# Optimization experiments

Hardware: AMD Instinct MI355X
Metric: run time of the kernel (lower is better)

Reference implementation:

```python
import jax, jax.numpy as jnp
import numpy as np

EPS = 1e-5
TEMP = 0.07
LARGE_NEG = -1e9


def mi_net(x, W1, g1, b1, W2, b2, Ws, lng, lnb):
    # x: (B, C, T). 1x1 convs == per-position channel projections.
    y = jnp.einsum('bct,oc->bot', x, W1)                      # conv1 (no bias)
    mu = y.mean(axis=(0, 2), keepdims=True)                   # BatchNorm2d, training-mode batch stats
    var = y.var(axis=(0, 2), keepdims=True)
    y = (y - mu) * jax.lax.rsqrt(var + EPS) * g1[None, :, None] + b1[None, :, None]
    y = jax.nn.relu(y)
    y = jnp.einsum('bot,po->bpt', y, W2) + b2[None, :, None]  # conv2 (bias)
    h = y + jnp.einsum('bct,oc->bot', x, Ws)                  # linear shortcut
    mu2 = h.mean(axis=1, keepdims=True)                       # LayerNorm over channel dim
    v2 = h.var(axis=1, keepdims=True)
    return (h - mu2) * jax.lax.rsqrt(v2 + EPS) * lng[None, :, None] + lnb[None, :, None]


def infonce(L, G):
    # L: (N, D, T) locals, G: (N, D) single global per sample (n_multis = 1)
    N, D, T = L.shape
    l_p = jnp.swapaxes(L, 1, 2)                               # (N, T, D)
    l_p = l_p / jnp.linalg.norm(l_p, axis=2, keepdims=True)
    g = G / jnp.linalg.norm(G, axis=1, keepdims=True)         # (N, D)
    u_p = (jnp.einsum('ntd,nd->nt', l_p, g) / TEMP)[:, :, None]   # (N, T, 1), positives scaled by temp
    # negatives: <global_i, local_{j,t}>; NOT divided by temperature (faithful to torch source)
    u_n = jnp.einsum('nd,mtd->nmt', g, l_p)                   # (N, N, T)
    eye = jnp.eye(N, dtype=bool)[:, :, None]
    u_n = jnp.where(eye, LARGE_NEG, u_n).reshape(N, N * T)    # mask self pairs
    logits = jnp.concatenate(
        [u_p, jnp.broadcast_to(u_n[:, None, :], (N, T, N * T))], axis=2)  # (N, T, 1+N*T)
    logp = jax.nn.log_softmax(logits, axis=2)
    return -logp[:, :, 0].mean()


def setup_inputs() -> dict:
    key = jax.random.key(0)
    ks = jax.random.split(key, 10)
    B, CL, CG, T, MI = 32, 1536, 192, 256, 512
    d = {
        'local_feat': jax.random.normal(ks[0], (B, CL, T), jnp.float32),
        'global_feat': jax.random.normal(ks[1], (B, CG), jnp.float32),
        # local_net params
        'lW1': jax.random.normal(ks[2], (MI, CL), jnp.float32) * 0.02,
        'lg1': jnp.ones((MI,), jnp.float32),
        'lb1': jnp.zeros((MI,), jnp.float32),
        'lW2': jax.random.normal(ks[3], (MI, MI), jnp.float32) * 0.02,
        'lb2': jnp.zeros((MI,), jnp.float32),
        'lWs': jax.random.normal(ks[4], (MI, CL), jnp.float32) * 0.02,
        'llng': jnp.ones((MI,), jnp.float32),
        'llnb': jnp.zeros((MI,), jnp.float32),
        # global_net params (global_channels != mi_units -> net exists)
        'gW1': jax.random.normal(ks[5], (MI, CG), jnp.float32) * 0.02,
        'gg1': jnp.ones((MI,), jnp.float32),
        'gb1': jnp.zeros((MI,), jnp.float32),
        'gW2': jax.random.normal(ks[6], (MI, MI), jnp.float32) * 0.02,
        'gb2': jnp.zeros((MI,), jnp.float32),
    }
    # shortcut with near-identity init (n_units >= n_input for global net)
    gWs = jax.random.uniform(ks[7], (MI, CG), jnp.float32, -0.01, 0.01)
    gWs = gWs.at[jnp.arange(CG), jnp.arange(CG)].set(1.0)
    d['gWs'] = gWs
    d['glng'] = jnp.ones((MI,), jnp.float32)
    d['glnb'] = jnp.zeros((MI,), jnp.float32)
    return d


def reference(local_feat, global_feat,
              lW1, lg1, lb1, lW2, lb2, lWs, llng, llnb,
              gW1, gg1, gb1, gW2, gb2, gWs, glng, glnb):
    L = mi_net(local_feat, lW1, lg1, lb1, lW2, lb2, lWs, llng, llnb)      # (B, MI, T)
    G = mi_net(global_feat[:, :, None], gW1, gg1, gb1, gW2, gb2, gWs, glng, glnb)[:, :, 0]  # (B, MI)
    return infonce(L, G)
```

## Files before the change

kernel.cpp:

```cpp
#include <hip/hip_runtime.h>

#define B 32
#define CL 1536
#define CG 192
#define T 256
#define MI 512
#define NPOS 8192
#define EPS 1e-5f
#define TEMP 0.07f

typedef __attribute__((ext_vector_type(8))) __bf16 bf16x8;
typedef __attribute__((ext_vector_type(4))) float f32x4;

__device__ __forceinline__ unsigned short f2bf(float f) {
  union { float f; unsigned u; } v; v.f = f;
  unsigned r = v.u + 0x7FFFu + ((v.u >> 16) & 1u);
  return (unsigned short)(r >> 16);
}
__device__ __forceinline__ float bf2f(unsigned short h) {
  union { unsigned u; float f; } v; v.u = ((unsigned)h) << 16;
  return v.f;
}

__device__ __forceinline__ float wave_sum(float v) {
#pragma unroll
  for (int off = 32; off > 0; off >>= 1) v += __shfl_xor(v, off, 64);
  return v;
}
__device__ __forceinline__ float block_sum(float v, float* rb) {
  v = wave_sum(v);
  __syncthreads();
  if ((threadIdx.x & 63) == 0) rb[threadIdx.x >> 6] = v;
  __syncthreads();
  return rb[0] + rb[1] + rb[2] + rb[3];
}

__global__ __launch_bounds__(256) void k_prep(
    const float* __restrict__ x, const float* __restrict__ lW1,
    const float* __restrict__ lWs, const float* __restrict__ lW2,
    const float* __restrict__ gx, const float* __restrict__ gW1,
    unsigned short* __restrict__ xT, unsigned short* __restrict__ Wc,
    unsigned short* __restrict__ W2b, float* __restrict__ y1g,
    float* __restrict__ bsum) {
  __shared__ float xs[64][65];
  const int bi = blockIdx.x, tid = threadIdx.x;
  if (bi < 1792) {
    int idx = (bi * 256 + tid) * 4;
    const float* src; unsigned short* dst;
    if (idx < 786432) { src = lW1 + idx; dst = Wc + idx; }
    else if (idx < 1572864) { src = lWs + (idx - 786432); dst = Wc + idx; }
    else { src = lW2 + (idx - 1572864); dst = W2b + (idx - 1572864); }
    float4 v = *(const float4*)src;
    ushort4 o = {f2bf(v.x), f2bf(v.y), f2bf(v.z), f2bf(v.w)};
    *(ushort4*)dst = o;
  } else if (bi < 4864) {
    int bi2 = bi - 1792;
    int b = bi2 / 96, rem = bi2 - b * 96;
    int c0 = (rem >> 2) * 64, t0 = (rem & 3) * 64;
    const float* xb = x + ((size_t)b * CL + c0) * T + t0;
#pragma unroll
    for (int i = 0; i < 4; i++) {
      int idx = tid + i * 256, c = idx >> 4, t4 = idx & 15;
      float4 v = *(const float4*)&xb[(size_t)c * T + t4 * 4];
      xs[c][t4 * 4 + 0] = v.x;
      xs[c][t4 * 4 + 1] = v.y;
      xs[c][t4 * 4 + 2] = v.z;
      xs[c][t4 * 4 + 3] = v.w;
    }
    __syncthreads();
    unsigned short* ob = xT + ((size_t)b * T + t0) * CL + c0;
#pragma unroll
    for (int half = 0; half < 2; half++) {
      int s = tid + half * 256;
      int t = s >> 3, kg = s & 7;
      unsigned short v[8];
#pragma unroll
      for (int j = 0; j < 8; j++) v[j] = f2bf(xs[kg * 8 + j][t]);
      uint4 o = {(unsigned)v[0] | ((unsigned)v[1] << 16),
                 (unsigned)v[2] | ((unsigned)v[3] << 16),
                 (unsigned)v[4] | ((unsigned)v[5] << 16),
                 (unsigned)v[6] | ((unsigned)v[7] << 16)};
      *(uint4*)&ob[(size_t)t * CL + kg * 8] = o;
    }
  } else if (bi < 4928) {
    int idx = (bi - 4864) * 256 + tid;
    int b = idx & 31, o = idx >> 5;
    float s = 0.f;
    for (int c = 0; c < CG; c++) s = fmaf(gx[b * CG + c], gW1[o * CG + c], s);
    y1g[o * 32 + b] = s;
  } else {
    float4 z = {0.f, 0.f, 0.f, 0.f};
    ((float4*)bsum)[tid] = z;
  }
}

__global__ __launch_bounds__(256, 2) void k_gemm1(
    const unsigned short* __restrict__ xT, const unsigned short* __restrict__ Wc,
    unsigned short* __restrict__ y1u, unsigned short* __restrict__ ysb,
    float* __restrict__ bsum, float* __restrict__ bsq,
    const float* __restrict__ y1g, const float* __restrict__ gg1,
    const float* __restrict__ gb1, const float* __restrict__ gW2,
    const float* __restrict__ gb2, const float* __restrict__ gx,
    const float* __restrict__ gWsc, float* __restrict__ hg) {
  const int tid = threadIdx.x, bi = blockIdx.x;
  if (bi >= 512) {
    __shared__ float gsc[512], gsh[512];
#pragma unroll
    for (int jj = 0; jj < 2; jj++) {
      int o = tid + jj * 256;
      float s = 0.f, s2 = 0.f;
      for (int b = 0; b < 32; b++) {
        float v = y1g[o * 32 + b];
        s += v; s2 = fmaf(v, v, s2);
      }
      float mu = s * (1.f / 32.f);
      float var = s2 * (1.f / 32.f) - mu * mu;
      float sc = gg1[o] * rsqrtf(var + EPS);
      gsc[o] = sc;
      gsh[o] = gb1[o] - mu * sc;
    }
    __syncthreads();
    int idx = (bi - 512) * 256 + tid;
    int b = idx & 31, p = idx >> 5;
    float s = gb2[p];
    for (int o = 0; o < MI; o++) {
      float v = fmaxf(fmaf(y1g[o * 32 + b], gsc[o], gsh[o]), 0.f);
      s = fmaf(v, gW2[(size_t)p * MI + o], s);
    }
    for (int c = 0; c < CG; c++) s = fmaf(gx[b * CG + c], gWsc[p * CG + c], s);
    hg[p * 32 + b] = s;
    return;
  }
  __shared__ __align__(16) unsigned short As[128 * 64];
  __shared__ __align__(16) unsigned short Bs[128 * 64];
  const int w = tid >> 6, lane = tid & 63;
  const int m0 = (bi & 63) * 128, o0 = (bi >> 6) * 128;
  const int wm = w & 1, wn = w >> 1;
  const int lm = lane & 15, q = lane >> 4;
  const int drow = lane >> 3;
  const int dchunk = (lane & 7) ^ drow;
  const int swz = lm & 7;
  f32x4 acc[4][4];
#pragma unroll
  for (int i = 0; i < 4; i++)
#pragma unroll
    for (int j = 0; j < 4; j++) acc[i][j] = f32x4{0.f, 0.f, 0.f, 0.f};

  const unsigned short* pa = xT + (size_t)(m0 + w * 32 + drow) * CL + dchunk * 8;
  const unsigned short* pb = Wc + (size_t)(o0 + w * 32 + drow) * CL + dchunk * 8;
  for (int k0 = 0; k0 < CL; k0 += 64) {
#pragma unroll
    for (int i = 0; i < 4; i++) {
      __builtin_amdgcn_global_load_lds(
          (const __attribute__((address_space(1))) void*)(pa + (size_t)i * 8 * CL + k0),
          (__attribute__((address_space(3))) void*)&As[(w * 32 + i * 8) * 64], 16, 0, 0);
      __builtin_amdgcn_global_load_lds(
          (const __attribute__((address_space(1))) void*)(pb + (size_t)i * 8 * CL + k0),
          (__attribute__((address_space(3))) void*)&Bs[(w * 32 + i * 8) * 64], 16, 0, 0);
    }
    __syncthreads();
#pragma unroll
    for (int kc = 0; kc < 2; kc++) {
      const int col = (((kc * 4 + q) ^ swz)) * 8;
      bf16x8 af[4], bfr[4];
#pragma unroll
      for (int mi = 0; mi < 4; mi++)
        af[mi] = *(const bf16x8*)&As[(wm * 64 + mi * 16 + lm) * 64 + col];
#pragma unroll
      for (int ni = 0; ni < 4; ni++)
        bfr[ni] = *(const bf16x8*)&Bs[(wn * 64 + ni * 16 + lm) * 64 + col];
#pragma unroll
      for (int mi = 0; mi < 4; mi++)
#pragma unroll
        for (int ni = 0; ni < 4; ni++)
          acc[mi][ni] = __builtin_amdgcn_mfma_f32_16x16x32_bf16(
              af[mi], bfr[ni], acc[mi][ni], 0, 0, 0);
    }
    __syncthreads();
  }
  const int row0 = m0 + wm * 64 + q * 4;
  const bool isY1 = (o0 < 512);
  unsigned short* dst = isY1 ? y1u : ysb;
  const int ob = isY1 ? o0 : o0 - 512;
#pragma unroll
  for (int mi = 0; mi < 4; mi++)
#pragma unroll
    for (int ni = 0; ni < 4; ni++) {
      int oc = ob + wn * 64 + ni * 16 + lm;
#pragma unroll
      for (int r = 0; r < 4; r++)
        dst[(size_t)(row0 + mi * 16 + r) * 512 + oc] = f2bf(acc[mi][ni][r]);
    }
  if (isY1) {
#pragma unroll
    for (int ni = 0; ni < 4; ni++) {
      float s = 0.f, s2 = 0.f;
#pragma unroll
      for (int mi = 0; mi < 4; mi++)
#pragma unroll
        for (int r = 0; r < 4; r++) {
          float v = acc[mi][ni][r];
          s += v; s2 = fmaf(v, v, s2);
        }
      s += __shfl_xor(s, 16, 64);  s2 += __shfl_xor(s2, 16, 64);
      s += __shfl_xor(s, 32, 64);  s2 += __shfl_xor(s2, 32, 64);
      if (q == 0) {
        int c = o0 + wn * 64 + ni * 16 + lm;
        atomicAdd(&bsum[c], s);
        atomicAdd(&bsq[c], s2);
      }
    }
  }
}

__global__ __launch_bounds__(256) void k_bnapp(
    const unsigned short* __restrict__ y1u, const float* __restrict__ bsum,
    const float* __restrict__ bsq, const float* __restrict__ lg1,
    const float* __restrict__ lb1, unsigned short* __restrict__ vv,
    const float* __restrict__ hg, const float* __restrict__ glng,
    const float* __restrict__ glnb, unsigned short* __restrict__ gnormb) {
  __shared__ float rb[4];
  const int bi = blockIdx.x, tid = threadIdx.x;
  if (bi >= 4096) {
    int b = bi - 4096;
    float v0 = hg[tid * 32 + b];
    float v1 = hg[(tid + 256) * 32 + b];
    float s = block_sum(v0 + v1, rb);
    float s2 = block_sum(fmaf(v0, v0, v1 * v1), rb);
    float mu = s * (1.f / MI);
    float var = s2 * (1.f / MI) - mu * mu;
    float rstd = rsqrtf(var + EPS);
    float L0 = fmaf((v0 - mu) * rstd, glng[tid], glnb[tid]);
    float L1 = fmaf((v1 - mu) * rstd, glng[tid + 256], glnb[tid + 256]);
    float n2 = block_sum(fmaf(L0, L0, L1 * L1), rb);
    float inv = rsqrtf(n2);
    gnormb[b * MI + tid] = f2bf(L0 * inv);
    gnormb[b * MI + tid + 256] = f2bf(L1 * inv);
    return;
  }
  int idx = (bi * 256 + tid) * 4;
  int o = idx & 511;
  ushort4 in = *(const ushort4*)&y1u[idx];
  float iv[4] = {bf2f(in.x), bf2f(in.y), bf2f(in.z), bf2f(in.w)};
  unsigned short ov[4];
#pragma unroll
  for (int j = 0; j < 4; j++) {
    float mu = bsum[o + j] * (1.f / NPOS);
    float var = bsq[o + j] * (1.f / NPOS) - mu * mu;
    float sc = lg1[o + j] * rsqrtf(var + EPS);
    float sh = lb1[o + j] - mu * sc;
    ov[j] = f2bf(fmaxf(fmaf(iv[j], sc, sh), 0.f));
  }
  ushort4 out = {ov[0], ov[1], ov[2], ov[3]};
  *(ushort4*)&vv[idx] = out;
}

__global__ __launch_bounds__(256, 2) void k_gemm2(
    const unsigned short* __restrict__ vv, const unsigned short* __restrict__ W2b,
    const float* __restrict__ b2, unsigned short* __restrict__ hb16) {
  __shared__ __align__(16) unsigned short As[128 * 64];
  __shared__ __align__(16) unsigned short Bs[128 * 64];
  const int tid = threadIdx.x, bi = blockIdx.x;
  const int w = tid >> 6, lane = tid & 63;
  const int m0 = (bi & 63) * 128, p0 = (bi >> 6) * 128;
  const int wm = w & 1, wn = w >> 1;
  const int lm = lane & 15, q = lane >> 4;
  const int drow = lane >> 3;
  const int dchunk = (lane & 7) ^ drow;
  const int swz = lm & 7;
  f32x4 acc[4][4];
#pragma unroll
  for (int i = 0; i < 4; i++)
#pragma unroll
    for (int j = 0; j < 4; j++) acc[i][j] = f32x4{0.f, 0.f, 0.f, 0.f};

  const unsigned short* pa = vv + (size_t)(m0 + w * 32 + drow) * 512 + dchunk * 8;
  const unsigned short* pb = W2b + (size_t)(p0 + w * 32 + drow) * 512 + dchunk * 8;
  for (int k0 = 0; k0 < 512; k0 += 64) {
#pragma unroll
    for (int i = 0; i < 4; i++) {
      __builtin_amdgcn_global_load_lds(
          (const __attribute__((address_space(1))) void*)(pa + (size_t)i * 8 * 512 + k0),
          (__attribute__((address_space(3))) void*)&As[(w * 32 + i * 8) * 64], 16, 0, 0);
      __builtin_amdgcn_global_load_lds(
          (const __attribute__((address_space(1))) void*)(pb + (size_t)i * 8 * 512 + k0),
          (__attribute__((address_space(3))) void*)&Bs[(w * 32 + i * 8) * 64], 16, 0, 0);
    }
    __syncthreads();
#pragma unroll
    for (int kc = 0; kc < 2; kc++) {
      const int col = (((kc * 4 + q) ^ swz)) * 8;
      bf16x8 af[4], bfr[4];
#pragma unroll
      for (int mi = 0; mi < 4; mi++)
        af[mi] = *(const bf16x8*)&As[(wm * 64 + mi * 16 + lm) * 64 + col];
#pragma unroll
      for (int ni = 0; ni < 4; ni++)
        bfr[ni] = *(const bf16x8*)&Bs[(wn * 64 + ni * 16 + lm) * 64 + col];
#pragma unroll
      for (int mi = 0; mi < 4; mi++)
#pragma unroll
        for (int ni = 0; ni < 4; ni++)
          acc[mi][ni] = __builtin_amdgcn_mfma_f32_16x16x32_bf16(
              af[mi], bfr[ni], acc[mi][ni], 0, 0, 0);
    }
    __syncthreads();
  }
  const int row0 = m0 + wm * 64 + q * 4;
#pragma unroll
  for (int ni = 0; ni < 4; ni++) {
    int p = p0 + wn * 64 + ni * 16 + lm;
    float bias = b2[p];
#pragma unroll
    for (int mi = 0; mi < 4; mi++)
#pragma unroll
      for (int r = 0; r < 4; r++) {
        size_t off = (size_t)(row0 + mi * 16 + r) * 512 + p;
        hb16[off] = f2bf(acc[mi][ni][r] + bias);
      }
  }
}

__global__ __launch_bounds__(256) void k_tail(
    const unsigned short* __restrict__ hb16, const unsigned short* __restrict__ ysb,
    const float* __restrict__ lng, const float* __restrict__ lnb,
    const unsigned short* __restrict__ gnormb,
    float* __restrict__ up, float* __restrict__ pmax, float* __restrict__ psum) {
  __shared__ __align__(16) unsigned short gs[32 * 512];
  __shared__ __align__(16) unsigned short Ls[32 * 512];
  __shared__ float Ured[4 * 1024];
  const int tid = threadIdx.x;
  const int w = tid >> 6, lane = tid & 63;
  const int r0 = blockIdx.x * 32;
  const int smp = r0 >> 8;
#pragma unroll
  for (int i = 0; i < 8; i++) {
    int e = (tid + i * 256) * 8;
    *(uint4*)&gs[e] = *(const uint4*)&gnormb[e];
  }
  float4 g0 = *(const float4*)&lng[lane * 8];
  float4 g1 = *(const float4*)&lng[lane * 8 + 4];
  float4 bb0 = *(const float4*)&lnb[lane * 8];
  float4 bb1 = *(const float4*)&lnb[lane * 8 + 4];
  float gg[8] = {g0.x, g0.y, g0.z, g0.w, g1.x, g1.y, g1.z, g1.w};
  float bz[8] = {bb0.x, bb0.y, bb0.z, bb0.w, bb1.x, bb1.y, bb1.z, bb1.w};
#pragma unroll
  for (int j = 0; j < 8; j++) {
    int rr = w * 8 + j;
    size_t off = (size_t)(r0 + rr) * 512 + lane * 8;
    uint4 hu = *(const uint4*)&hb16[off];
    uint4 yu = *(const uint4*)&ysb[off];
    unsigned short hv[8] = {
        (unsigned short)(hu.x & 0xffff), (unsigned short)(hu.x >> 16),
        (unsigned short)(hu.y & 0xffff), (unsigned short)(hu.y >> 16),
        (unsigned short)(hu.z & 0xffff), (unsigned short)(hu.z >> 16),
        (unsigned short)(hu.w & 0xffff), (unsigned short)(hu.w >> 16)};
    unsigned short yv[8] = {
        (unsigned short)(yu.x & 0xffff), (unsigned short)(yu.x >> 16),
        (unsigned short)(yu.y & 0xffff), (unsigned short)(yu.y >> 16),
        (unsigned short)(yu.z & 0xffff), (unsigned short)(yu.z >> 16),
        (unsigned short)(yu.w & 0xffff), (unsigned short)(yu.w >> 16)};
    float v[8];
    float s = 0.f, s2 = 0.f;
#pragma unroll
    for (int k = 0; k < 8; k++) {
      v[k] = bf2f(hv[k]) + bf2f(yv[k]);
      s += v[k]; s2 = fmaf(v[k], v[k], s2);
    }
    s = wave_sum(s);
    s2 = wave_sum(s2);
    float mu = s * (1.f / MI);
    float var = s2 * (1.f / MI) - mu * mu;
    float rstd = rsqrtf(var + EPS);
    float L[8], n2 = 0.f;
#pragma unroll
    for (int k = 0; k < 8; k++) {
      L[k] = fmaf((v[k] - mu) * rstd, gg[k], bz[k]);
      n2 = fmaf(L[k], L[k], n2);
    }
    n2 = wave_sum(n2);
    float inv = rsqrtf(n2);
    unsigned short* orow = &Ls[rr * 512 + lane * 8];
    ushort4 o0 = {f2bf(L[0] * inv), f2bf(L[1] * inv), f2bf(L[2] * inv), f2bf(L[3] * inv)};
    ushort4 o1 = {f2bf(L[4] * inv), f2bf(L[5] * inv), f2bf(L[6] * inv), f2bf(L[7] * inv)};
    *(ushort4*)orow = o0;
    *(ushort4*)(orow + 4) = o1;
  }
  __syncthreads();
  const int lm = lane & 15, q = lane >> 4;
  f32x4 acc[2][2];
#pragma unroll
  for (int i = 0; i < 2; i++)
#pragma unroll
    for (int j = 0; j < 2; j++) acc[i][j] = f32x4{0.f, 0.f, 0.f, 0.f};
#pragma unroll
  for (int kk = 0; kk < 4; kk++) {
    int k0 = w * 128 + kk * 32 + q * 8;
    bf16x8 af[2], bfr[2];
#pragma unroll
    for (int mi = 0; mi < 2; mi++)
      af[mi] = *(const bf16x8*)&gs[(mi * 16 + lm) * 512 + k0];
#pragma unroll
    for (int ni = 0; ni < 2; ni++)
      bfr[ni] = *(const bf16x8*)&Ls[(ni * 16 + lm) * 512 + k0];
#pragma unroll
    for (int mi = 0; mi < 2; mi++)
#pragma unroll
      for (int ni = 0; ni < 2; ni++)
        acc[mi][ni] = __builtin_amdgcn_mfma_f32_16x16x32_bf16(
            af[mi], bfr[ni], acc[mi][ni], 0, 0, 0);
  }
#pragma unroll
  for (int mi = 0; mi < 2; mi++)
#pragma unroll
    for (int ni = 0; ni < 2; ni++)
#pragma unroll
      for (int r = 0; r < 4; r++) {
        int m = mi * 16 + q * 4 + r, n = ni * 16 + lm;
        Ured[w * 1024 + m * 32 + n] = acc[mi][ni][r];
      }
  __syncthreads();
  float u[4];
#pragma unroll
  for (int j = 0; j < 4; j++) {
    int idx = tid * 4 + j;
    u[j] = Ured[idx] + Ured[1024 + idx] + Ured[2048 + idx] + Ured[3072 + idx];
  }
  __syncthreads();
#pragma unroll
  for (int j = 0; j < 4; j++) Ured[tid * 4 + j] = u[j];
  int m = (tid * 4) >> 5;
  if (m == smp) {
#pragma unroll
    for (int j = 0; j < 4; j++)
      up[r0 + ((tid * 4 + j) & 31)] = u[j] * (1.f / TEMP);
  }
  __syncthreads();
  if (tid < 32) {
    float mx = -1e30f, s = 0.f;
    if (tid != smp) {
      for (int n = 0; n < 32; n++) mx = fmaxf(mx, Ured[tid * 32 + n]);
      for (int n = 0; n < 32; n++) s += expf(Ured[tid * 32 + n] - mx);
    }
    pmax[tid * 256 + blockIdx.x] = mx;
    psum[tid * 256 + blockIdx.x] = s;
  }
}

__global__ __launch_bounds__(256) void k_loss(
    const float* __restrict__ up, const float* __restrict__ pmax,
    const float* __restrict__ psum, float* __restrict__ out) {
  __shared__ float rb[4];
  __shared__ float red[32][8];
  __shared__ float Ms[32], Ss[32];
  const int tid = threadIdx.x;
  const int n = tid >> 3, j = tid & 7;
  float mx = -1e30f;
  for (int c = j * 32; c < j * 32 + 32; c++) mx = fmaxf(mx, pmax[n * 256 + c]);
  red[n][j] = mx;
  __syncthreads();
  if (j == 0) {
    float M = -1e30f;
#pragma unroll
    for (int k = 0; k < 8; k++) M = fmaxf(M, red[n][k]);
    Ms[n] = M;
  }
  __syncthreads();
  float M = Ms[n];
  float s = 0.f;
  for (int c = j * 32; c < j * 32 + 32; c++)
    s += psum[n * 256 + c] * expf(pmax[n * 256 + c] - M);
  __syncthreads();
  red[n][j] = s;
  __syncthreads();
  if (j == 0) {
    float S = 0.f;
#pragma unroll
    for (int k = 0; k < 8; k++) S += red[n][k];
    Ss[n] = S;
  }
  __syncthreads();
  float acc = 0.f;
  for (int i = tid; i < NPOS; i += 256) {
    int nn = i >> 8;
    float upv = up[i];
    float Mn = Ms[nn], Sn = Ss[nn];
    float mx2 = fmaxf(upv, Mn);
    float lse = mx2 + logf(expf(upv - mx2) + Sn * expf(Mn - mx2));
    acc += lse - upv;
  }
  acc = block_sum(acc, rb);
  if (tid == 0) out[0] = acc * (1.f / NPOS);
}

extern "C" void kernel_launch(void* const* d_in, const int* in_sizes, int n_in,
                              void* d_out, int out_size, void* d_ws, size_t ws_size,
                              hipStream_t stream) {
  (void)in_sizes; (void)n_in; (void)out_size; (void)ws_size;
  const float* x    = (const float*)d_in[0];
  const float* gx   = (const float*)d_in[1];
  const float* lW1  = (const float*)d_in[2];
  const float* lg1  = (const float*)d_in[3];
  const float* lb1  = (const float*)d_in[4];
  const float* lW2  = (const float*)d_in[5];
  const float* lb2  = (const float*)d_in[6];
  const float* lWs  = (const float*)d_in[7];
  const float* llng = (const float*)d_in[8];
  const float* llnb = (const float*)d_in[9];
  const float* gW1  = (const float*)d_in[10];
  const float* gg1  = (const float*)d_in[11];
  const float* gb1  = (const float*)d_in[12];
  const float* gW2  = (const float*)d_in[13];
  const float* gb2  = (const float*)d_in[14];
  const float* gWs  = (const float*)d_in[15];
  const float* glng = (const float*)d_in[16];
  const float* glnb = (const float*)d_in[17];

  char* wsb = (char*)d_ws;
  unsigned short* xT     = (unsigned short*)(wsb);
  unsigned short* Wc     = (unsigned short*)(wsb + 25165824);
  unsigned short* W2b    = (unsigned short*)(wsb + 28311552);
  unsigned short* y1u    = (unsigned short*)(wsb + 28835840);
  unsigned short* ysb    = (unsigned short*)(wsb + 37224448);
  unsigned short* vv     = (unsigned short*)(wsb + 45613056);
  unsigned short* hb16   = (unsigned short*)(wsb + 54001664);
  float* bsum            = (float*)(wsb + 62390272);
  float* bsq             = (float*)(wsb + 62392320);
  float* y1g             = (float*)(wsb + 62394368);
  float* hg              = (float*)(wsb + 62459904);
  unsigned short* gnormb = (unsigned short*)(wsb + 62525440);
  float* up              = (float*)(wsb + 62558208);
  float* pmax            = (float*)(wsb + 62590976);
  float* psum            = (float*)(wsb + 62623744);

  k_prep<<<dim3(4929), 256, 0, stream>>>(x, lW1, lWs, lW2, gx, gW1, xT, Wc, W2b,
                                         y1g, bsum);
  k_gemm1<<<dim3(576), 256, 0, stream>>>(xT, Wc, y1u, ysb, bsum, bsq,
                                         y1g, gg1, gb1, gW2, gb2, gx, gWs, hg);
  k_bnapp<<<dim3(4128), 256, 0, stream>>>(y1u, bsum, bsq, lg1, lb1, vv,
                                          hg, glng, glnb, gnormb);
  k_gemm2<<<dim3(256), 256, 0, stream>>>(vv, W2b, lb2, hb16);
  k_tail<<<dim3(256), 256, 0, stream>>>(hb16, ysb, llng, llnb, gnormb,
                                        up, pmax, psum);
  k_loss<<<dim3(1), 256, 0, stream>>>(up, pmax, psum, (float*)d_out);
}
```

Baseline: 217.3 us.

## Switch first local GEMM to FP8 inputs with scaled weights

Converts the transposed local features and the concatenated conv1/shortcut weights to FP8 (weights pre-scaled by 64) instead of bf16, and runs the first GEMM with fp8 MFMA over K-tiles of 128. The results are rescaled before the bf16 store and the batch-stat accumulation. This halves the bytes written by prep and read by the GEMM and uses the higher-throughput fp8 matrix path. It costs accuracy, since the inputs are unnormalized Gaussians and the weights are small, so FP8 rounding could shift the loss beyond tolerance.

New measurement: 217.4 us. No clear change (+0.1%).

```diff
diff --git a/kernel.cpp b/kernel.cpp
--- a/kernel.cpp
+++ b/kernel.cpp
@@ -8,9 +8,12 @@
 #define NPOS 8192
 #define EPS 1e-5f
 #define TEMP 0.07f
+#define WSCALE 64.0f
+#define INV_WSCALE (1.0f / 64.0f)
 
 typedef __attribute__((ext_vector_type(8))) __bf16 bf16x8;
 typedef __attribute__((ext_vector_type(4))) float f32x4;
+typedef long i64;
 
 __device__ __forceinline__ unsigned short f2bf(float f) {
   union { float f; unsigned u; } v; v.f = f;
@@ -21,6 +24,10 @@
   union { unsigned u; float f; } v; v.u = ((unsigned)h) << 16;
   return v.f;
 }
+__device__ __forceinline__ unsigned pk4_fp8(float a, float b, float c, float d) {
+  int lo = __builtin_amdgcn_cvt_pk_fp8_f32(a, b, 0, false);
+  return (unsigned)__builtin_amdgcn_cvt_pk_fp8_f32(c, d, lo, true);
+}
 
 __device__ __forceinline__ float wave_sum(float v) {
 #pragma unroll
@@ -39,20 +46,22 @@
     const float* __restrict__ x, const float* __restrict__ lW1,
     const float* __restrict__ lWs, const float* __restrict__ lW2,
     const float* __restrict__ gx, const float* __restrict__ gW1,
-    unsigned short* __restrict__ xT, unsigned short* __restrict__ Wc,
+    unsigned char* __restrict__ x8, unsigned char* __restrict__ Wc8,
     unsigned short* __restrict__ W2b, float* __restrict__ y1g,
     float* __restrict__ bsum) {
   __shared__ float xs[64][65];
   const int bi = blockIdx.x, tid = threadIdx.x;
-  if (bi < 1792) {
+  if (bi < 1536) {
     int idx = (bi * 256 + tid) * 4;
-    const float* src; unsigned short* dst;
-    if (idx < 786432) { src = lW1 + idx; dst = Wc + idx; }
-    else if (idx < 1572864) { src = lWs + (idx - 786432); dst = Wc + idx; }
-    else { src = lW2 + (idx - 1572864); dst = W2b + (idx - 1572864); }
+    const float* src = (idx < 786432) ? (lW1 + idx) : (lWs + idx - 786432);
     float4 v = *(const float4*)src;
+    *(unsigned*)&Wc8[idx] = pk4_fp8(v.x * WSCALE, v.y * WSCALE,
+                                    v.z * WSCALE, v.w * WSCALE);
+  } else if (bi < 1792) {
+    int idx = ((bi - 1536) * 256 + tid) * 4;
+    float4 v = *(const float4*)&lW2[idx];
     ushort4 o = {f2bf(v.x), f2bf(v.y), f2bf(v.z), f2bf(v.w)};
-    *(ushort4*)dst = o;
+    *(ushort4*)&W2b[idx] = o;
   } else if (bi < 4864) {
     int bi2 = bi - 1792;
     int b = bi2 / 96, rem = bi2 - b * 96;
@@ -68,19 +77,16 @@
       xs[c][t4 * 4 + 3] = v.w;
     }
     __syncthreads();
-    unsigned short* ob = xT + ((size_t)b * T + t0) * CL + c0;
-#pragma unroll
-    for (int half = 0; half < 2; half++) {
-      int s = tid + half * 256;
-      int t = s >> 3, kg = s & 7;
-      unsigned short v[8];
-#pragma unroll
-      for (int j = 0; j < 8; j++) v[j] = f2bf(xs[kg * 8 + j][t]);
-      uint4 o = {(unsigned)v[0] | ((unsigned)v[1] << 16),
-                 (unsigned)v[2] | ((unsigned)v[3] << 16),
-                 (unsigned)v[4] | ((unsigned)v[5] << 16),
-                 (unsigned)v[6] | ((unsigned)v[7] << 16)};
-      *(uint4*)&ob[(size_t)t * CL + kg * 8] = o;
+    unsigned char* ob = x8 + ((size_t)b * T + t0) * CL + c0;
+    {
+      int t = tid >> 2, cg = tid & 3;
+      unsigned u[4];
+#pragma unroll
+      for (int k = 0; k < 4; k++)
+        u[k] = pk4_fp8(xs[cg * 16 + k * 4 + 0][t], xs[cg * 16 + k * 4 + 1][t],
+                       xs[cg * 16 + k * 4 + 2][t], xs[cg * 16 + k * 4 + 3][t]);
+      uint4 o = {u[0], u[1], u[2], u[3]};
+      *(uint4*)&ob[(size_t)t * CL + cg * 16] = o;
     }
   } else if (bi < 4928) {
     int idx = (bi - 4864) * 256 + tid;
@@ -95,7 +101,7 @@
 }
 
 __global__ __launch_bounds__(256, 2) void k_gemm1(
-    const unsigned short* __restrict__ xT, const unsigned short* __restrict__ Wc,
+    const unsigned char* __restrict__ x8, const unsigned char* __restrict__ Wc8,
     unsigned short* __restrict__ y1u, unsigned short* __restrict__ ysb,
     float* __restrict__ bsum, float* __restrict__ bsq,
     const float* __restrict__ y1g, const float* __restrict__ gg1,
@@ -131,8 +137,8 @@
     hg[p * 32 + b] = s;
     return;
   }
-  __shared__ __align__(16) unsigned short As[128 * 64];
-  __shared__ __align__(16) unsigned short Bs[128 * 64];
+  __shared__ __align__(16) unsigned char As[128 * 128];
+  __shared__ __align__(16) unsigned char Bs[128 * 128];
   const int w = tid >> 6, lane = tid & 63;
   const int m0 = (bi & 63) * 128, o0 = (bi >> 6) * 128;
   const int wm = w & 1, wn = w >> 1;
@@ -140,40 +146,41 @@
   const int drow = lane >> 3;
   const int dchunk = (lane & 7) ^ drow;
   const int swz = lm & 7;
+  const int qh = q >> 1, qb = (q & 1) * 8;
   f32x4 acc[4][4];
 #pragma unroll
   for (int i = 0; i < 4; i++)
 #pragma unroll
     for (int j = 0; j < 4; j++) acc[i][j] = f32x4{0.f, 0.f, 0.f, 0.f};
 
-  const unsigned short* pa = xT + (size_t)(m0 + w * 32 + drow) * CL + dchunk * 8;
-  const unsigned short* pb = Wc + (size_t)(o0 + w * 32 + drow) * CL + dchunk * 8;
-  for (int k0 = 0; k0 < CL; k0 += 64) {
+  const unsigned char* pa = x8 + (size_t)(m0 + w * 32 + drow) * CL + dchunk * 16;
+  const unsigned char* pb = Wc8 + (size_t)(o0 + w * 32 + drow) * CL + dchunk * 16;
+  for (int k0 = 0; k0 < CL; k0 += 128) {
 #pragma unroll
     for (int i = 0; i < 4; i++) {
       __builtin_amdgcn_global_load_lds(
           (const __attribute__((address_space(1))) void*)(pa + (size_t)i * 8 * CL + k0),
-          (__attribute__((address_space(3))) void*)&As[(w * 32 + i * 8) * 64], 16, 0, 0);
+          (__attribute__((address_space(3))) void*)&As[(w * 32 + i * 8) * 128], 16, 0, 0);
       __builtin_amdgcn_global_load_lds(
           (const __attribute__((address_space(1))) void*)(pb + (size_t)i * 8 * CL + k0),
-          (__attribute__((address_space(3))) void*)&Bs[(w * 32 + i * 8) * 64], 16, 0, 0);
+          (__attribute__((address_space(3))) void*)&Bs[(w * 32 + i * 8) * 128], 16, 0, 0);
     }
     __syncthreads();
 #pragma unroll
-    for (int kc = 0; kc < 2; kc++) {
-      const int col = (((kc * 4 + q) ^ swz)) * 8;
-      bf16x8 af[4], bfr[4];
+    for (int kc = 0; kc < 4; kc++) {
+      const int col = (((kc * 2 + qh) ^ swz)) * 16 + qb;
+      i64 af[4], bfr[4];
 #pragma unroll
       for (int mi = 0; mi < 4; mi++)
-        af[mi] = *(const bf16x8*)&As[(wm * 64 + mi * 16 + lm) * 64 + col];
+        af[mi] = *(const i64*)&As[(wm * 64 + mi * 16 + lm) * 128 + col];
 #pragma unroll
       for (int ni = 0; ni < 4; ni++)
-        bfr[ni] = *(const bf16x8*)&Bs[(wn * 64 + ni * 16 + lm) * 64 + col];
+        bfr[ni] = *(const i64*)&Bs[(wn * 64 + ni * 16 + lm) * 128 + col];
 #pragma unroll
       for (int mi = 0; mi < 4; mi++)
 #pragma unroll
         for (int ni = 0; ni < 4; ni++)
-          acc[mi][ni] = __builtin_amdgcn_mfma_f32_16x16x32_bf16(
+          acc[mi][ni] = __builtin_amdgcn_mfma_f32_16x16x32_fp8_fp8(
               af[mi], bfr[ni], acc[mi][ni], 0, 0, 0);
     }
     __syncthreads();
@@ -189,7 +196,8 @@
       int oc = ob + wn * 64 + ni * 16 + lm;
 #pragma unroll
       for (int r = 0; r < 4; r++)
-        dst[(size_t)(row0 + mi * 16 + r) * 512 + oc] = f2bf(acc[mi][ni][r]);
+        dst[(size_t)(row0 + mi * 16 + r) * 512 + oc] =
+            f2bf(acc[mi][ni][r] * INV_WSCALE);
     }
   if (isY1) {
 #pragma unroll
@@ -199,7 +207,7 @@
       for (int mi = 0; mi < 4; mi++)
 #pragma unroll
         for (int r = 0; r < 4; r++) {
-          float v = acc[mi][ni][r];
+          float v = acc[mi][ni][r] * INV_WSCALE;
           s += v; s2 = fmaf(v, v, s2);
         }
       s += __shfl_xor(s, 16, 64);  s2 += __shfl_xor(s2, 16, 64);
@@ -517,25 +525,25 @@
   const float* glnb = (const float*)d_in[17];
 
   char* wsb = (char*)d_ws;
-  unsigned short* xT     = (unsigned short*)(wsb);
-  unsigned short* Wc     = (unsigned short*)(wsb + 25165824);
-  unsigned short* W2b    = (unsigned short*)(wsb + 28311552);
-  unsigned short* y1u    = (unsigned short*)(wsb + 28835840);
-  unsigned short* ysb    = (unsigned short*)(wsb + 37224448);
-  unsigned short* vv     = (unsigned short*)(wsb + 45613056);
-  unsigned short* hb16   = (unsigned short*)(wsb + 54001664);
-  float* bsum            = (float*)(wsb + 62390272);
-  float* bsq             = (float*)(wsb + 62392320);
-  float* y1g             = (float*)(wsb + 62394368);
-  float* hg              = (float*)(wsb + 62459904);
-  unsigned short* gnormb = (unsigned short*)(wsb + 62525440);
-  float* up              = (float*)(wsb + 62558208);
-  float* pmax            = (float*)(wsb + 62590976);
-  float* psum            = (float*)(wsb + 62623744);
-
-  k_prep<<<dim3(4929), 256, 0, stream>>>(x, lW1, lWs, lW2, gx, gW1, xT, Wc, W2b,
+  unsigned char* x8      = (unsigned char*)(wsb);
+  unsigned char* Wc8     = (unsigned char*)(wsb + 12582912);
+  unsigned short* W2b    = (unsigned short*)(wsb + 14155776);
+  unsigned short* y1u    = (unsigned short*)(wsb + 14680064);
+  unsigned short* ysb    = (unsigned short*)(wsb + 23068672);
+  unsigned short* vv     = (unsigned short*)(wsb + 31457280);
+  unsigned short* hb16   = (unsigned short*)(wsb + 39845888);
+  float* bsum            = (float*)(wsb + 48234496);
+  float* bsq             = (float*)(wsb + 48236544);
+  float* y1g             = (float*)(wsb + 48238592);
+  float* hg              = (float*)(wsb + 48304128);
+  unsigned short* gnormb = (unsigned short*)(wsb + 48369664);
+  float* up              = (float*)(wsb + 48402432);
+  float* pmax            = (float*)(wsb + 48435200);
+  float* psum            = (float*)(wsb + 48467968);
+
+  k_prep<<<dim3(4929), 256, 0, stream>>>(x, lW1, lWs, lW2, gx, gW1, x8, Wc8, W2b,
                                          y1g, bsum);
-  k_gemm1<<<dim3(576), 256, 0, stream>>>(xT, Wc, y1u, ysb, bsum, bsq,
+  k_gemm1<<<dim3(576), 256, 0, stream>>>(x8, Wc8, y1u, ysb, bsum, bsq,
                                          y1g, gg1, gb1, gW2, gb2, gx, gWs, hg);
   k_bnapp<<<dim3(4128), 256, 0, stream>>>(y1u, bsum, bsq, lg1, lb1, vv,
                                           hg, glng, glnb, gnormb);
```
